# Kernel optimization log

Hardware: AMD Instinct MI355X
Metric: run time of the kernel (lower is better)

Reference implementation:

```python
import jax, jax.numpy as jnp
import numpy as np
import math

INC, OUTC, NPARAM = 64, 128, 8
B, D, H, W = 2, 12, 48, 48
BN_EPS = 1e-5


def _p_n(num_param):
    # replicates LDConv_3D._get_p_n kernel-point layout
    base = round(math.sqrt(num_param))
    dep = round(num_param ** (1.0 / 3.0))
    row = num_param // (base * dep)
    mod = num_param % (base * dep)
    z, x, y = np.meshgrid(np.arange(dep), np.arange(row), np.arange(base), indexing='ij')
    z, x, y = z.ravel(), x.ravel(), y.ravel()
    if mod > 0:
        mz, mx, my = np.meshgrid(np.arange(dep, dep + 1), np.arange(row, row + 1), np.arange(mod), indexing='ij')
        z = np.concatenate([z, mz.ravel()])
        x = np.concatenate([x, mx.ravel()])
        y = np.concatenate([y, my.ravel()])
    return (jnp.asarray(z, jnp.float32), jnp.asarray(x, jnp.float32), jnp.asarray(y, jnp.float32))


def _conv3d(x, w, stride, pad):
    return jax.lax.conv_general_dilated(x, w, window_strides=stride, padding=pad,
                                        dimension_numbers=('NCDHW', 'OIDHW', 'NCDHW'))


def setup_inputs() -> dict:
    key = jax.random.key(0)
    ks = jax.random.split(key, 5)
    x = jax.random.normal(ks[0], (B, INC, D, H, W), jnp.float32)
    w_p = jax.random.normal(ks[1], (3 * NPARAM, INC, 3, 3, 3), jnp.float32) * 0.01
    b_p = jax.random.normal(ks[2], (3 * NPARAM,), jnp.float32) * 0.01
    w_conv = jax.random.normal(ks[3], (OUTC, INC, NPARAM, 1, 1), jnp.float32) * (1.0 / math.sqrt(INC * NPARAM))
    gamma = jnp.ones((OUTC,), jnp.float32)
    beta = jnp.zeros((OUTC,), jnp.float32)
    return {'x': x, 'w_p': w_p, 'b_p': b_p, 'w_conv': w_conv, 'gamma': gamma, 'beta': beta}


def reference(x, w_p, b_p, w_conv, gamma, beta):
    b, c, d, h, w = x.shape
    N = NPARAM
    # learned offsets: (b, 3N, d, h, w)
    offset = _conv3d(x, w_p, (1, 1, 1), [(1, 1), (1, 1), (1, 1)]) + b_p[None, :, None, None, None]
    off = jnp.transpose(offset, (0, 2, 3, 4, 1))  # b d h w 3N
    oz, ox, oy = off[..., :N], off[..., N:2 * N], off[..., 2 * N:]
    pnz, pnx, pny = _p_n(N)
    # sampling positions p = p_0 + p_n + offset  (stride=1)
    pz = oz + jnp.arange(d, dtype=jnp.float32)[None, :, None, None, None] + pnz
    px = ox + jnp.arange(h, dtype=jnp.float32)[None, None, :, None, None] + pnx
    py = oy + jnp.arange(w, dtype=jnp.float32)[None, None, None, :, None] + pny
    # integer corner coords (detached floor, clamped)
    fz = jnp.floor(jax.lax.stop_gradient(pz))
    fx = jnp.floor(jax.lax.stop_gradient(px))
    fy = jnp.floor(jax.lax.stop_gradient(py))
    qltz = jnp.clip(fz, 0, d - 1)
    qltx = jnp.clip(fx, 0, h - 1)
    qlty = jnp.clip(fy, 0, w - 1)
    qrbz = jnp.clip(fz + 1, 0, d - 1)
    qrbx = jnp.clip(fx + 1, 0, h - 1)
    qrby = jnp.clip(fy + 1, 0, w - 1)
    # clamped continuous positions
    pzc = jnp.clip(pz, 0, d - 1)
    pxc = jnp.clip(px, 0, h - 1)
    pyc = jnp.clip(py, 0, w - 1)
    # trilinear weights for the 4 gathered corners (as in source)
    g_lt = (1 + (qltz - pzc)) * (1 + (qltx - pxc)) * (1 + (qlty - pyc))
    g_rb = (1 - (qrbz - pzc)) * (1 - (qrbx - pxc)) * (1 - (qrby - pyc))
    g_lb = (1 + (qltz - pzc)) * (1 - (qrbx - pxc)) * (1 + (qlty - pyc))
    g_rt = (1 - (qrbz - pzc)) * (1 + (qltx - pxc)) * (1 - (qrby - pyc))
    x_flat = x.reshape(b, c, d * h * w)
    def gath(qz, qx, qy):
        idx = (qz.astype(jnp.int32) * (h * w) + qx.astype(jnp.int32) * w + qy.astype(jnp.int32)).reshape(b, -1)
        g = jax.vmap(lambda xf, i: jnp.take(xf, i, axis=1))(x_flat, idx)
        return g.reshape(b, c, d, h, w, N)
    x_lt = gath(qltz, qltx, qlty)
    x_rb = gath(qrbz, qrbx, qrby)
    x_lb = gath(qltz, qrbx, qlty)
    x_rt = gath(qrbz, qltx, qrby)
    x_off = (g_lt[:, None] * x_lt + g_rb[:, None] * x_rb +
             g_lb[:, None] * x_lb + g_rt[:, None] * x_rt)  # b c d h w N
    # rearrange 'b c d h w n -> b c (d n) h w'
    x_off = jnp.transpose(x_off, (0, 1, 2, 5, 3, 4)).reshape(b, c, d * N, h, w)
    out = _conv3d(x_off, w_conv, (N, 1, 1), [(0, 0), (0, 0), (0, 0)])  # b outc d h w
    # BatchNorm3d (training-mode batch stats, biased var) + SiLU
    mean = jnp.mean(out, axis=(0, 2, 3, 4), keepdims=True)
    var = jnp.mean((out - mean) ** 2, axis=(0, 2, 3, 4), keepdims=True)
    out = (out - mean) * jax.lax.rsqrt(var + BN_EPS)
    out = out * gamma[None, :, None, None, None] + beta[None, :, None, None, None]
    return jax.nn.silu(out)
```

## Files before the change

### kernel.cpp

```cpp
#include <hip/hip_runtime.h>
#include <math.h>

#define BATCH 2
#define INC   64
#define OUTCH 128
#define NP    8
#define DD    12
#define HH    48
#define WW    48
#define HW    (HH*WW)
#define DHW   (DD*HW)
#define SPTS  (BATCH*DHW)
#define KDIM  (INC*NP)
#define NELEM (BATCH*OUTCH*DHW)
#define VSTRIDE 516

#define WS_W2B  0
#define WS_W3   32768
#define WS_PART 88064
#define WS_XT   90112
#define WS_OFF  1859584

typedef __attribute__((ext_vector_type(8))) short short8;
typedef __attribute__((ext_vector_type(4))) float floatx4;

__device__ __forceinline__ ushort f2bf(float f) {
    unsigned u = __float_as_uint(f);
    unsigned r = (u + 0x7fffu + ((u >> 16) & 1u)) >> 16;
    return (ushort)r;
}

__device__ __forceinline__ unsigned interp2(unsigned a, unsigned b, unsigned c, unsigned d,
                                            float g0, float g1, float g2, float g3) {
    float vl = g0 * __uint_as_float(a << 16) + g1 * __uint_as_float(b << 16)
             + g2 * __uint_as_float(c << 16) + g3 * __uint_as_float(d << 16);
    float vh = g0 * __uint_as_float(a & 0xffff0000u) + g1 * __uint_as_float(b & 0xffff0000u)
             + g2 * __uint_as_float(c & 0xffff0000u) + g3 * __uint_as_float(d & 0xffff0000u);
    return (unsigned)f2bf(vl) | ((unsigned)f2bf(vh) << 16);
}

__global__ __launch_bounds__(256) void k_prep_w2b(const float* __restrict__ wc,
                                                  ushort* __restrict__ w2b) {
    int t = blockIdx.x * 256 + threadIdx.x;
    int j  = t & 7;
    int oc = (t >> 3) & 127;
    int kq = t >> 10;
    int e  = kq * 8 + j;
    int ic = e & 63;
    int n  = e >> 6;
    w2b[t] = f2bf(wc[(oc * INC + ic) * NP + n]);
}

__global__ __launch_bounds__(256) void k_prep_w3(const float* __restrict__ wp,
                                                 float* __restrict__ w3c) {
    int t = blockIdx.x * 256 + threadIdx.x;
    int ch = t & 31;
    int iu = t >> 5;
    w3c[t] = (ch < 24) ? wp[ch * 1728 + iu] : 0.f;
}

__global__ __launch_bounds__(256) void k_transpose_x(const float* __restrict__ x,
                                                     unsigned* __restrict__ xTu) {
    int t = blockIdx.x * 256 + threadIdx.x;
    int icp = t & 31;
    int sg  = t >> 5;
    int b   = sg / DHW;
    int s   = sg - b * DHW;
    const float* xb = x + (size_t)b * INC * DHW + s;
    float v0 = xb[(2 * icp) * DHW];
    float v1 = xb[(2 * icp + 1) * DHW];
    xTu[t] = (unsigned)f2bf(v0) | ((unsigned)f2bf(v1) << 16);
}

__global__ __launch_bounds__(256, 4) void k_conv(const float* __restrict__ x,
                                                 const float* __restrict__ w3c,
                                                 const float* __restrict__ bp,
                                                 float* __restrict__ off) {
    int t    = threadIdx.x;
    int lane = t & 63;
    int hgq  = __builtin_amdgcn_readfirstlane(t >> 6);
    int q0 = blockIdx.x * 128;
    int bb = q0 / DHW;
    int s0 = q0 - bb * DHW;
    int dp = s0 / HW;
    int rp = s0 - dp * HW + 2 * lane;
    int hp = rp / WW;
    int c0 = rp - hp * WW;
    const float* xb = x + (size_t)bb * INC * DHW;
    const float* wbase = w3c + hgq * 6;

    int rAo = (hp > 0      ? hp - 1 : 0     ) * WW;
    int rMo = hp * WW;
    int rBo = (hp < HH - 1 ? hp + 1 : HH - 1) * WW;
    int oL = (c0 > 0)  ? c0 - 2 : 0;
    int oM = c0;
    int oR = (c0 < 46) ? c0 + 2 : 46;

    float rm0 = (hp > 0)      ? 1.f : 0.f;
    float rm2 = (hp < HH - 1) ? 1.f : 0.f;
    float clm = (c0 > 0)      ? 1.f : 0.f;
    float crm = (c0 < 46)     ? 1.f : 0.f;
    float m0[9], m1[9];
    #pragma unroll
    for (int kx = 0; kx < 3; ++kx) {
        float rmv = kx == 0 ? rm0 : (kx == 1 ? 1.f : rm2);
        #pragma unroll
        for (int ky = 0; ky < 3; ++ky) {
            int u = kx * 3 + ky;
            m0[u] = rmv * (ky == 0 ? clm : 1.f);
            m1[u] = rmv * (ky == 2 ? crm : 1.f);
        }
    }

    float acc[2][6];
    #pragma unroll
    for (int c = 0; c < 6; ++c) { acc[0][c] = bp[hgq * 6 + c]; acc[1][c] = bp[hgq * 6 + c]; }

    #pragma unroll 1
    for (int kz = 0; kz < 3; ++kz) {
        int z = dp + kz - 1;
        if ((unsigned)z >= DD) continue;
        const float* xz = xb + z * HW;
        #pragma unroll 2
        for (int ic = 0; ic < 64; ++ic) {
            const float* xp = xz + (size_t)ic * DHW;
            float2 LA = *reinterpret_cast<const float2*>(xp + rAo + oL);
            float2 MA = *reinterpret_cast<const float2*>(xp + rAo + oM);
            float2 RA = *reinterpret_cast<const float2*>(xp + rAo + oR);
            float2 LM = *reinterpret_cast<const float2*>(xp + rMo + oL);
            float2 MM = *reinterpret_cast<const float2*>(xp + rMo + oM);
            float2 RM = *reinterpret_cast<const float2*>(xp + rMo + oR);
            float2 LB = *reinterpret_cast<const float2*>(xp + rBo + oL);
            float2 MB = *reinterpret_cast<const float2*>(xp + rBo + oM);
            float2 RB = *reinterpret_cast<const float2*>(xp + rBo + oR);
            const float* wk = wbase + (ic * 27 + kz * 9) * 32;
            #pragma unroll
            for (int kx = 0; kx < 3; ++kx) {
                float tv[4];
                if (kx == 0)      { tv[0] = LA.y; tv[1] = MA.x; tv[2] = MA.y; tv[3] = RA.x; }
                else if (kx == 1) { tv[0] = LM.y; tv[1] = MM.x; tv[2] = MM.y; tv[3] = RM.x; }
                else              { tv[0] = LB.y; tv[1] = MB.x; tv[2] = MB.y; tv[3] = RB.x; }
                #pragma unroll
                for (int ky = 0; ky < 3; ++ky) {
                    int u = kx * 3 + ky;
                    const float* w6 = wk + u * 32;
                    float xv0 = tv[ky]     * m0[u];
                    float xv1 = tv[ky + 1] * m1[u];
                    #pragma unroll
                    for (int c = 0; c < 6; ++c) {
                        acc[0][c] = fmaf(xv0, w6[c], acc[0][c]);
                        acc[1][c] = fmaf(xv1, w6[c], acc[1][c]);
                    }
                }
            }
        }
    }

    float2* o0 = reinterpret_cast<float2*>(off + (size_t)(q0 + 2 * lane) * 24 + hgq * 6);
    o0[0] = make_float2(acc[0][0], acc[0][1]);
    o0[1] = make_float2(acc[0][2], acc[0][3]);
    o0[2] = make_float2(acc[0][4], acc[0][5]);
    float2* o1 = reinterpret_cast<float2*>(off + (size_t)(q0 + 2 * lane + 1) * 24 + hgq * 6);
    o1[0] = make_float2(acc[1][0], acc[1][1]);
    o1[1] = make_float2(acc[1][2], acc[1][3]);
    o1[2] = make_float2(acc[1][4], acc[1][5]);
}

__global__ __launch_bounds__(256, 4) void k_fused(const unsigned* __restrict__ xTu,
                                                  const float* __restrict__ off,
                                                  const ushort* __restrict__ w2b,
                                                  float* __restrict__ out) {
    __shared__ __align__(16) ushort sVb[32 * VSTRIDE];
    __shared__ __align__(16) ushort4 sMiP[256];
    __shared__ __align__(16) float4  sMgP[256];

    int t  = threadIdx.x;
    int q0 = blockIdx.x * 32;
    int bb = q0 / DHW;

    {
        int i = t >> 3, n = t & 7;
        int s = q0 + i - bb * DHW;
        int d = s / HW; int r = s - d * HW; int h = r / WW; int w = r - h * WW;

        const float* op = off + (size_t)(q0 + i) * 24;
        float a0 = op[n];
        float a1 = op[8 + n];
        float a2 = op[16 + n];

        float pnz = (n < 6) ? (float)(n / 3) : 2.f;
        float pnx = (n < 6) ? 0.f : 1.f;
        float pny = (n < 6) ? (float)(n % 3) : (float)(n - 6);
        float pz = a0 + (float)d + pnz;
        float px = a1 + (float)h + pnx;
        float py = a2 + (float)w + pny;
        float fz = floorf(pz), fx = floorf(px), fy = floorf(py);
        float z0 = fminf(fmaxf(fz, 0.f), DD - 1.f), z1 = fminf(fmaxf(fz + 1.f, 0.f), DD - 1.f);
        float x0 = fminf(fmaxf(fx, 0.f), HH - 1.f), x1 = fminf(fmaxf(fx + 1.f, 0.f), HH - 1.f);
        float y0 = fminf(fmaxf(fy, 0.f), WW - 1.f), y1 = fminf(fmaxf(fy + 1.f, 0.f), WW - 1.f);
        float pzc = fminf(fmaxf(pz, 0.f), DD - 1.f);
        float pxc = fminf(fmaxf(px, 0.f), HH - 1.f);
        float pyc = fminf(fmaxf(py, 0.f), WW - 1.f);
        float wz0 = 1.f + z0 - pzc, wz1 = 1.f - z1 + pzc;
        float wx0 = 1.f + x0 - pxc, wx1 = 1.f - x1 + pxc;
        float wy0 = 1.f + y0 - pyc, wy1 = 1.f - y1 + pyc;
        float c0 = wz0 * wy0, c1 = wz1 * wy1;
        int iz0 = (int)z0, iz1 = (int)z1, ix0 = (int)x0, ix1 = (int)x1, iy0 = (int)y0, iy1 = (int)y1;
        ushort i0 = (ushort)((iz0 * HH + ix0) * WW + iy0);
        ushort i1 = (ushort)((iz0 * HH + ix1) * WW + iy0);
        ushort i2 = (ushort)((iz1 * HH + ix0) * WW + iy1);
        ushort i3 = (ushort)((iz1 * HH + ix1) * WW + iy1);
        sMiP[t] = make_ushort4(i0, i1, i2, i3);
        sMgP[t] = make_float4(c0 * wx0, c0 * wx1, c1 * wx0, c1 * wx1);
    }
    __syncthreads();

    {
        const unsigned* xTb = xTu + (size_t)bb * DHW * 32;
        unsigned* sVbU = reinterpret_cast<unsigned*>(sVb);
        int tk = t >> 3, ch8 = t & 7;

        #pragma unroll 4
        for (int cc = 0; cc < 8; ++cc) {
            int gt = cc * 32 + tk;
            ushort4 mi = sMiP[gt];
            float4  mg = sMgP[gt];
            uint4 A = *reinterpret_cast<const uint4*>(xTb + (size_t)mi.x * 32 + ch8 * 4);
            uint4 B = *reinterpret_cast<const uint4*>(xTb + (size_t)mi.y * 32 + ch8 * 4);
            uint4 C = *reinterpret_cast<const uint4*>(xTb + (size_t)mi.z * 32 + ch8 * 4);
            uint4 D = *reinterpret_cast<const uint4*>(xTb + (size_t)mi.w * 32 + ch8 * 4);
            unsigned o0 = interp2(A.x, B.x, C.x, D.x, mg.x, mg.y, mg.z, mg.w);
            unsigned o1 = interp2(A.y, B.y, C.y, D.y, mg.x, mg.y, mg.z, mg.w);
            unsigned o2 = interp2(A.z, B.z, C.z, D.z, mg.x, mg.y, mg.z, mg.w);
            unsigned o3 = interp2(A.w, B.w, C.w, D.w, mg.x, mg.y, mg.z, mg.w);
            int ii = gt >> 3, nn = gt & 7;
            int wb = ii * (VSTRIDE / 2) + nn * 32 + ch8 * 4;
            *reinterpret_cast<uint2*>(&sVbU[wb])     = make_uint2(o0, o1);
            *reinterpret_cast<uint2*>(&sVbU[wb + 2]) = make_uint2(o2, o3);
        }
    }
    __syncthreads();

    {
        int lane = t & 63;
        int wid  = t >> 6;
        int l16  = lane & 15;
        int q    = lane >> 4;
        int ocA0 = (wid * 2) * 16 + l16;
        const ushort* A0 = w2b + ((q * 128) + ocA0) * 8;
        const ushort* A1 = A0 + 16 * 8;
        const ushort* B0 = sVb + l16 * VSTRIDE + q * 8;
        const ushort* B1 = B0 + 16 * VSTRIDE;

        floatx4 c00 = {0.f, 0.f, 0.f, 0.f};
        floatx4 c01 = {0.f, 0.f, 0.f, 0.f};
        floatx4 c10 = {0.f, 0.f, 0.f, 0.f};
        floatx4 c11 = {0.f, 0.f, 0.f, 0.f};

        #pragma unroll 4
        for (int kt = 0; kt < 16; ++kt) {
            short8 af0 = *reinterpret_cast<const short8*>(A0 + kt * 4096);
            short8 af1 = *reinterpret_cast<const short8*>(A1 + kt * 4096);
            short8 bf0 = *reinterpret_cast<const short8*>(B0 + kt * 32);
            short8 bf1 = *reinterpret_cast<const short8*>(B1 + kt * 32);
            c00 = __builtin_amdgcn_mfma_f32_16x16x32_bf16(af0, bf0, c00, 0, 0, 0);
            c01 = __builtin_amdgcn_mfma_f32_16x16x32_bf16(af0, bf1, c01, 0, 0, 0);
            c10 = __builtin_amdgcn_mfma_f32_16x16x32_bf16(af1, bf0, c10, 0, 0, 0);
            c11 = __builtin_amdgcn_mfma_f32_16x16x32_bf16(af1, bf1, c11, 0, 0, 0);
        }

        int s0 = q0 - bb * DHW;
        float* outb = out + (size_t)bb * OUTCH * DHW + s0;
        int ocRow = (wid * 2) * 16 + q * 4;
        #pragma unroll
        for (int rg = 0; rg < 4; ++rg) {
            outb[(ocRow + rg) * DHW + l16]            = c00[rg];
            outb[(ocRow + rg) * DHW + 16 + l16]       = c01[rg];
            outb[(ocRow + 16 + rg) * DHW + l16]       = c10[rg];
            outb[(ocRow + 16 + rg) * DHW + 16 + l16]  = c11[rg];
        }
    }
}

__global__ __launch_bounds__(256) void k_stats_partial(const float* __restrict__ out,
                                                       float* __restrict__ part) {
    int c = blockIdx.x >> 3;
    int j = blockIdx.x & 7;
    int b = j & 1, quarter = j >> 1;
    const float4* p = reinterpret_cast<const float4*>(
        out + (size_t)(b * OUTCH + c) * DHW + quarter * (DHW / 4));
    float sum = 0.f, ss = 0.f;
    for (int s = threadIdx.x; s < DHW / 16; s += 256) {
        float4 v = p[s];
        sum += v.x + v.y + v.z + v.w;
        ss = fmaf(v.x, v.x, ss); ss = fmaf(v.y, v.y, ss);
        ss = fmaf(v.z, v.z, ss); ss = fmaf(v.w, v.w, ss);
    }
    __shared__ float r1[256], r2[256];
    r1[threadIdx.x] = sum; r2[threadIdx.x] = ss;
    __syncthreads();
    for (int ofs = 128; ofs > 0; ofs >>= 1) {
        if (threadIdx.x < ofs) {
            r1[threadIdx.x] += r1[threadIdx.x + ofs];
            r2[threadIdx.x] += r2[threadIdx.x + ofs];
        }
        __syncthreads();
    }
    if (threadIdx.x == 0) {
        part[c * 8 + j]             = r1[0];
        part[OUTCH * 8 + c * 8 + j] = r2[0];
    }
}

__global__ __launch_bounds__(256) void k_bn_silu(float* __restrict__ out,
                                                 const float* __restrict__ part,
                                                 const float* __restrict__ gamma,
                                                 const float* __restrict__ beta) {
    int t = blockIdx.x * 256 + threadIdx.x;
    int base = t * 4;
    int c = (base / DHW) & 127;
    float sum = 0.f, ss = 0.f;
    #pragma unroll
    for (int j = 0; j < 8; ++j) {
        sum += part[c * 8 + j];
        ss  += part[OUTCH * 8 + c * 8 + j];
    }
    const float inv_n = 1.f / (float)(BATCH * DHW);
    float mean = sum * inv_n;
    float var  = ss * inv_n - mean * mean;
    float sc   = gamma[c] * rsqrtf(var + 1e-5f);
    float bi   = beta[c] - mean * sc;
    float4 v = *reinterpret_cast<float4*>(&out[base]);
    float y0 = fmaf(v.x, sc, bi);
    float y1 = fmaf(v.y, sc, bi);
    float y2 = fmaf(v.z, sc, bi);
    float y3 = fmaf(v.w, sc, bi);
    v.x = y0 / (1.f + expf(-y0));
    v.y = y1 / (1.f + expf(-y1));
    v.z = y2 / (1.f + expf(-y2));
    v.w = y3 / (1.f + expf(-y3));
    *reinterpret_cast<float4*>(&out[base]) = v;
}

extern "C" void kernel_launch(void* const* d_in, const int* in_sizes, int n_in,
                              void* d_out, int out_size, void* d_ws, size_t ws_size,
                              hipStream_t stream) {
    const float* x     = (const float*)d_in[0];
    const float* wp    = (const float*)d_in[1];
    const float* bp    = (const float*)d_in[2];
    const float* wc    = (const float*)d_in[3];
    const float* gamma = (const float*)d_in[4];
    const float* beta  = (const float*)d_in[5];
    float* out = (float*)d_out;
    float* ws  = (float*)d_ws;

    ushort*   w2b  = reinterpret_cast<ushort*>(ws + WS_W2B);
    float*    w3c  = ws + WS_W3;
    float*    part = ws + WS_PART;
    unsigned* xTu  = reinterpret_cast<unsigned*>(ws + WS_XT);
    float*    off  = ws + WS_OFF;

    k_prep_w2b<<<65536 / 256, 256, 0, stream>>>(wc, w2b);
    k_prep_w3<<<55296 / 256, 256, 0, stream>>>(wp, w3c);
    k_conv<<<SPTS / 128, 256, 0, stream>>>(x, w3c, bp, off);
    k_transpose_x<<<(SPTS * 32) / 256, 256, 0, stream>>>(x, xTu);
    k_fused<<<SPTS / 32, 256, 0, stream>>>(xTu, off, w2b, out);
    k_stats_partial<<<OUTCH * 8, 256, 0, stream>>>(out, part);
    k_bn_silu<<<(NELEM / 4) / 256, 256, 0, stream>>>(out, part, gamma, beta);
}
```

Before: 249.5 us.

## Fuse BN statistics into GEMM epilogue and tile x transpose through LDS

Result: no change. 250.7 us (+0.5%).

```diff
diff --git a/kernel.cpp b/kernel.cpp
--- a/kernel.cpp
+++ b/kernel.cpp
@@ -20,6 +20,8 @@
 #define WS_PART 88064
 #define WS_XT   90112
 #define WS_OFF  1859584
+#define WS_PSQ  3186688
+#define WS_PF   3203072
 
 typedef __attribute__((ext_vector_type(8))) short short8;
 typedef __attribute__((ext_vector_type(4))) float floatx4;
@@ -52,8 +54,10 @@
 }
 
 __global__ __launch_bounds__(256) void k_prep_w3(const float* __restrict__ wp,
-                                                 float* __restrict__ w3c) {
+                                                 float* __restrict__ w3c,
+                                                 float* __restrict__ psq) {
     int t = blockIdx.x * 256 + threadIdx.x;
+    if (t < 16384) psq[t] = 0.f;
     int ch = t & 31;
     int iu = t >> 5;
     w3c[t] = (ch < 24) ? wp[ch * 1728 + iu] : 0.f;
@@ -61,15 +65,31 @@
 
 __global__ __launch_bounds__(256) void k_transpose_x(const float* __restrict__ x,
                                                      unsigned* __restrict__ xTu) {
-    int t = blockIdx.x * 256 + threadIdx.x;
+    __shared__ float sX[64 * 65];
+    int t  = threadIdx.x;
+    int q0 = blockIdx.x * 64;
+    int bb = q0 / DHW;
+    int s0 = q0 - bb * DHW;
+    const float* xb = x + (size_t)bb * INC * DHW + s0;
+
+    int si  = t & 63;
+    int icL = t >> 6;
+    #pragma unroll
+    for (int k = 0; k < 16; ++k) {
+        int ic = k * 4 + icL;
+        sX[ic * 65 + si] = xb[(size_t)ic * DHW + si];
+    }
+    __syncthreads();
+
     int icp = t & 31;
-    int sg  = t >> 5;
-    int b   = sg / DHW;
-    int s   = sg - b * DHW;
-    const float* xb = x + (size_t)b * INC * DHW + s;
-    float v0 = xb[(2 * icp) * DHW];
-    float v1 = xb[(2 * icp + 1) * DHW];
-    xTu[t] = (unsigned)f2bf(v0) | ((unsigned)f2bf(v1) << 16);
+    int sjb = t >> 5;
+    #pragma unroll
+    for (int pass = 0; pass < 8; ++pass) {
+        int sj = pass * 8 + sjb;
+        float v0 = sX[(2 * icp)     * 65 + sj];
+        float v1 = sX[(2 * icp + 1) * 65 + sj];
+        xTu[(size_t)(q0 + sj) * 32 + icp] = (unsigned)f2bf(v0) | ((unsigned)f2bf(v1) << 16);
+    }
 }
 
 __global__ __launch_bounds__(256, 4) void k_conv(const float* __restrict__ x,
@@ -169,7 +189,8 @@
 __global__ __launch_bounds__(256, 4) void k_fused(const unsigned* __restrict__ xTu,
                                                   const float* __restrict__ off,
                                                   const ushort* __restrict__ w2b,
-                                                  float* __restrict__ out) {
+                                                  float* __restrict__ out,
+                                                  float* __restrict__ psq) {
     __shared__ __align__(16) ushort sVb[32 * VSTRIDE];
     __shared__ __align__(16) ushort4 sMiP[256];
     __shared__ __align__(16) float4  sMgP[256];
@@ -279,52 +300,52 @@
             outb[(ocRow + 16 + rg) * DHW + l16]       = c10[rg];
             outb[(ocRow + 16 + rg) * DHW + 16 + l16]  = c11[rg];
         }
-    }
-}
-
-__global__ __launch_bounds__(256) void k_stats_partial(const float* __restrict__ out,
-                                                       float* __restrict__ part) {
-    int c = blockIdx.x >> 3;
-    int j = blockIdx.x & 7;
-    int b = j & 1, quarter = j >> 1;
-    const float4* p = reinterpret_cast<const float4*>(
-        out + (size_t)(b * OUTCH + c) * DHW + quarter * (DHW / 4));
-    float sum = 0.f, ss = 0.f;
-    for (int s = threadIdx.x; s < DHW / 16; s += 256) {
-        float4 v = p[s];
-        sum += v.x + v.y + v.z + v.w;
-        ss = fmaf(v.x, v.x, ss); ss = fmaf(v.y, v.y, ss);
-        ss = fmaf(v.z, v.z, ss); ss = fmaf(v.w, v.w, ss);
-    }
-    __shared__ float r1[256], r2[256];
-    r1[threadIdx.x] = sum; r2[threadIdx.x] = ss;
-    __syncthreads();
-    for (int ofs = 128; ofs > 0; ofs >>= 1) {
-        if (threadIdx.x < ofs) {
-            r1[threadIdx.x] += r1[threadIdx.x + ofs];
-            r2[threadIdx.x] += r2[threadIdx.x + ofs];
-        }
-        __syncthreads();
-    }
-    if (threadIdx.x == 0) {
-        part[c * 8 + j]             = r1[0];
-        part[OUTCH * 8 + c * 8 + j] = r2[0];
-    }
+
+        int slot = blockIdx.x & 63;
+        #pragma unroll
+        for (int rg = 0; rg < 4; ++rg) {
+            float sA = c00[rg] + c01[rg];
+            float qA = c00[rg] * c00[rg] + c01[rg] * c01[rg];
+            float sB = c10[rg] + c11[rg];
+            float qB = c10[rg] * c10[rg] + c11[rg] * c11[rg];
+            #pragma unroll
+            for (int m = 1; m < 16; m <<= 1) {
+                sA += __shfl_xor(sA, m);
+                qA += __shfl_xor(qA, m);
+                sB += __shfl_xor(sB, m);
+                qB += __shfl_xor(qB, m);
+            }
+            if (l16 == 0) {
+                int chA = ocRow + rg;
+                int chB = chA + 16;
+                atomicAdd(&psq[chA * 64 + slot], sA);
+                atomicAdd(&psq[8192 + chA * 64 + slot], qA);
+                atomicAdd(&psq[chB * 64 + slot], sB);
+                atomicAdd(&psq[8192 + chB * 64 + slot], qB);
+            }
+        }
+    }
+}
+
+__global__ __launch_bounds__(256) void k_reduce(const float* __restrict__ psq,
+                                                float* __restrict__ partF) {
+    int t = threadIdx.x;
+    const float* src = psq + (size_t)t * 64;
+    float s = 0.f;
+    #pragma unroll
+    for (int i = 0; i < 64; ++i) s += src[i];
+    partF[t] = s;
 }
 
 __global__ __launch_bounds__(256) void k_bn_silu(float* __restrict__ out,
-                                                 const float* __restrict__ part,
+                                                 const float* __restrict__ partF,
                                                  const float* __restrict__ gamma,
                                                  const float* __restrict__ beta) {
     int t = blockIdx.x * 256 + threadIdx.x;
     int base = t * 4;
     int c = (base / DHW) & 127;
-    float sum = 0.f, ss = 0.f;
-    #pragma unroll
-    for (int j = 0; j < 8; ++j) {
-        sum += part[c * 8 + j];
-        ss  += part[OUTCH * 8 + c * 8 + j];
-    }
+    float sum = partF[c];
+    float ss  = partF[128 + c];
     const float inv_n = 1.f / (float)(BATCH * DHW);
     float mean = sum * inv_n;
     float var  = ss * inv_n - mean * mean;
@@ -356,15 +377,16 @@
 
     ushort*   w2b  = reinterpret_cast<ushort*>(ws + WS_W2B);
     float*    w3c  = ws + WS_W3;
-    float*    part = ws + WS_PART;
     unsigned* xTu  = reinterpret_cast<unsigned*>(ws + WS_XT);
     float*    off  = ws + WS_OFF;
+    float*    psq  = ws + WS_PSQ;
+    float*    pF   = ws + WS_PF;
 
     k_prep_w2b<<<65536 / 256, 256, 0, stream>>>(wc, w2b);
-    k_prep_w3<<<55296 / 256, 256, 0, stream>>>(wp, w3c);
+    k_prep_w3<<<55296 / 256, 256, 0, stream>>>(wp, w3c, psq);
     k_conv<<<SPTS / 128, 256, 0, stream>>>(x, w3c, bp, off);
-    k_transpose_x<<<(SPTS * 32) / 256, 256, 0, stream>>>(x, xTu);
-    k_fused<<<SPTS / 32, 256, 0, stream>>>(xTu, off, w2b, out);
-    k_stats_partial<<<OUTCH * 8, 256, 0, stream>>>(out, part);
-    k_bn_silu<<<(NELEM / 4) / 256, 256, 0, stream>>>(out, part, gamma, beta);
-}
+    k_transpose_x<<<SPTS / 64, 256, 0, stream>>>(x, xTu);
+    k_fused<<<SPTS / 32, 256, 0, stream>>>(xTu, off, w2b, out, psq);
+    k_reduce<<<1, 256, 0, stream>>>(psq, pF);
+    k_bn_silu<<<(NELEM / 4) / 256, 256, 0, stream>>>(out, pF, gamma, beta);
+}
```
